# Optimization experiments

Hardware: AMD Instinct MI355X
Metric: run time of the kernel (lower is better)

The kernel has to match this reference:

```python
import jax, jax.numpy as jnp
import numpy as np

B, S, D = 4, 2048, 1024
H, HD = 16, 64  # num_heads, head_dim = qkv_features // num_heads


def setup_inputs() -> dict:
  key = jax.random.key(0)
  ks = jax.random.split(key, 11)
  s = 0.02
  return {
    'inputs_q': jax.random.normal(ks[0], (B, S, D), jnp.float32),
    'inputs_k': jax.random.normal(ks[1], (B, S, D), jnp.float32),
    'inputs_v': jax.random.normal(ks[2], (B, S, D), jnp.float32),
    # LinearGeneral kernels: [in_features, num_heads, head_dim]
    'Wq': jax.random.normal(ks[3], (D, H, HD), jnp.float32) * s,
    'bq': jnp.zeros((H, HD), jnp.float32),
    'Wk': jax.random.normal(ks[4], (D, H, HD), jnp.float32) * s,
    'bk': jnp.zeros((H, HD), jnp.float32),
    'Wv': jax.random.normal(ks[5], (D, H, HD), jnp.float32) * s,
    'bv': jnp.zeros((H, HD), jnp.float32),
    # output LinearGeneral kernel: [num_heads, head_dim, out_features]
    'Wo': jax.random.normal(ks[6], (H, HD, D), jnp.float32) * s,
    'bo': jnp.zeros((D,), jnp.float32),
  }


def reference(inputs_q, inputs_k, inputs_v, Wq, bq, Wk, bk, Wv, bv, Wo, bo):
  # q/k/v projections -> [B, S, H, HD]
  q = jnp.einsum('bsf,fhd->bshd', inputs_q, Wq) + bq
  k = jnp.einsum('bsf,fhd->bshd', inputs_k, Wk) + bk
  v = jnp.einsum('bsf,fhd->bshd', inputs_v, Wv) + bv
  # scaled dot-product attention (naive full softmax, as in the module)
  depth = q.shape[-1]
  q = q / jnp.sqrt(jnp.asarray(depth, q.dtype))
  attn = jnp.einsum('bqhd,bkhd->bhqk', q, k)  # [B, H, S, S]
  attn = jax.nn.softmax(attn, axis=-1)
  x = jnp.einsum('bhqk,bkhd->bqhd', attn, v)  # [B, S, H, HD]
  # output projection -> [B, S, D]
  out = jnp.einsum('bqhd,hdo->bqo', x, Wo) + bo
  return out
```

## Files before the change

kernel.cpp:

```cpp
#include <hip/hip_runtime.h>


typedef __attribute__((ext_vector_type(4))) float f32x4;
typedef __attribute__((ext_vector_type(8))) short short8;
typedef unsigned short u16;
typedef unsigned int u32;

__device__ __forceinline__ u16 f2bf(float f) {
  u32 u = __builtin_bit_cast(u32, f);
  u += 0x7fffu + ((u >> 16) & 1u);
  return (u16)(u >> 16);
}

__device__ __forceinline__ void gload16(const u16* g, u16* l) {
  __builtin_amdgcn_global_load_lds((const __attribute__((address_space(1))) void*)g,
                                   (__attribute__((address_space(3))) void*)l, 16, 0, 0);
}

__global__ __launch_bounds__(256) void cvt_f32_bf16_3(const float* __restrict__ a,
                                                      const float* __restrict__ b,
                                                      const float* __restrict__ c,
                                                      u16* __restrict__ oa,
                                                      u16* __restrict__ ob,
                                                      u16* __restrict__ oc) {
  const float* in = blockIdx.y == 0 ? a : (blockIdx.y == 1 ? b : c);
  u16* out = blockIdx.y == 0 ? oa : (blockIdx.y == 1 ? ob : oc);
  int i = blockIdx.x * 256 + threadIdx.x;
  float4 v = ((const float4*)in)[i];
  ushort4 o;
  o.x = f2bf(v.x); o.y = f2bf(v.y); o.z = f2bf(v.z); o.w = f2bf(v.w);
  ((ushort4*)out)[i] = o;
}

__global__ __launch_bounds__(256) void transpose_w4(const float* __restrict__ s0,
                                                    const float* __restrict__ s1,
                                                    const float* __restrict__ s2,
                                                    const float* __restrict__ s3,
                                                    u16* __restrict__ d0,
                                                    u16* __restrict__ d1,
                                                    u16* __restrict__ d2,
                                                    u16* __restrict__ d3) {
  const float* src = blockIdx.z == 0 ? s0 : (blockIdx.z == 1 ? s1 : (blockIdx.z == 2 ? s2 : s3));
  u16* dst = blockIdx.z == 0 ? d0 : (blockIdx.z == 1 ? d1 : (blockIdx.z == 2 ? d2 : d3));
  __shared__ float t[64][65];
  const int bx = blockIdx.x * 64;
  const int by = blockIdx.y * 64;
  const int tid = threadIdx.x;
  const int c4 = (tid & 15) * 4, r = tid >> 4;
#pragma unroll
  for (int i = 0; i < 4; ++i) {
    int row = r + i * 16;
    float4 v = *(const float4*)&src[(size_t)(by + row) * 1024 + bx + c4];
    t[row][c4] = v.x; t[row][c4 + 1] = v.y; t[row][c4 + 2] = v.z; t[row][c4 + 3] = v.w;
  }
  __syncthreads();
#pragma unroll
  for (int i = 0; i < 4; ++i) {
    int nrow = r + i * 16;
    ushort4 o;
    o.x = f2bf(t[c4 + 0][nrow]); o.y = f2bf(t[c4 + 1][nrow]);
    o.z = f2bf(t[c4 + 2][nrow]); o.w = f2bf(t[c4 + 3][nrow]);
    *(ushort4*)&dst[(size_t)(bx + nrow) * 1024 + by + c4] = o;
  }
}

template <int EPI>
__global__ __launch_bounds__(256) void gemm_k1024(const u16* __restrict__ A,
                                                  const u16* __restrict__ Bt,
                                                  const float* __restrict__ bias,
                                                  void* __restrict__ outp) {
  __shared__ u16 lds[2 * 8192];
  u16* ldsA = lds;
  u16* ldsB = lds + 8192;
  const int tid = threadIdx.x, ln = tid & 63, wv = tid >> 6;
  const int wr = wv >> 1, wc = wv & 1;
  const int lq = ln & 15, g = ln >> 4;
  const int m0 = blockIdx.y * 128, n0 = blockIdx.x * 128;
  f32x4 acc[4][4] = {};

  for (int kt = 0; kt < 16; ++kt) {
    const int k0 = kt * 64;
#pragma unroll
    for (int c = 0; c < 4; ++c) {
      int chunk = c * 256 + wv * 64 + ln;
      int row = chunk >> 3, cc = chunk & 7;
      gload16(A + (size_t)(m0 + row) * 1024 + k0 + ((cc ^ (row & 7)) << 3),
              ldsA + (c * 256 + wv * 64) * 8);
    }
#pragma unroll
    for (int c = 0; c < 4; ++c) {
      int chunk = c * 256 + wv * 64 + ln;
      int row = chunk >> 3, cc = chunk & 7;
      gload16(Bt + (size_t)(n0 + row) * 1024 + k0 + ((cc ^ (row & 7)) << 3),
              ldsB + (c * 256 + wv * 64) * 8);
    }
    __syncthreads();
#pragma unroll
    for (int ks = 0; ks < 2; ++ks) {
      short8 af[4], bf[4];
#pragma unroll
      for (int m = 0; m < 4; ++m) {
        int rA = wr * 64 + m * 16 + lq;
        int cc = (ks * 4 + g) ^ (rA & 7);
        af[m] = *(const short8*)&ldsA[rA * 64 + cc * 8];
      }
#pragma unroll
      for (int n = 0; n < 4; ++n) {
        int rB = wc * 64 + n * 16 + lq;
        int cc = (ks * 4 + g) ^ (rB & 7);
        bf[n] = *(const short8*)&ldsB[rB * 64 + cc * 8];
      }
#pragma unroll
      for (int m = 0; m < 4; ++m)
#pragma unroll
        for (int n = 0; n < 4; ++n)
          acc[m][n] = __builtin_amdgcn_mfma_f32_16x16x32_bf16(af[m], bf[n], acc[m][n], 0, 0, 0);
    }
    __syncthreads();
  }

#pragma unroll
  for (int m = 0; m < 4; ++m) {
#pragma unroll
    for (int n = 0; n < 4; ++n) {
      const int row = m0 + wr * 64 + m * 16 + g * 4;
      const int col = n0 + wc * 64 + n * 16 + lq;
      const float bb = bias[col];
      if constexpr (EPI == 0 || EPI == 1) {
        u16* O = (u16*)outp;
        int b = row >> 11, s = row & 2047, h = col >> 6, d = col & 63;
        size_t base = ((size_t)(b * 16 + h) * 2048 + s) * 64 + d;
#pragma unroll
        for (int j = 0; j < 4; ++j) {
          float v = acc[m][n][j] + bb;
          if constexpr (EPI == 0) v *= 0.18033688f;
          O[base + (size_t)j * 64] = f2bf(v);
        }
      } else if constexpr (EPI == 2) {
        u16* O = (u16*)outp;
        int b = row >> 11, s = row & 2047, h = col >> 6, d = col & 63;
        ushort4 pk;
        pk.x = f2bf(acc[m][n][0] + bb); pk.y = f2bf(acc[m][n][1] + bb);
        pk.z = f2bf(acc[m][n][2] + bb); pk.w = f2bf(acc[m][n][3] + bb);
        *(ushort4*)&O[((size_t)(b * 16 + h) * 64 + d) * 2048 + s] = pk;
      } else {
        float* O = (float*)outp;
#pragma unroll
        for (int j = 0; j < 4; ++j) O[(size_t)(row + j) * 1024 + col] = acc[m][n][j] + bb;
      }
    }
  }
}

__global__ __launch_bounds__(256) void attn_kernel(const u16* __restrict__ Q,
                                                   const u16* __restrict__ K,
                                                   const u16* __restrict__ Vt,
                                                   u16* __restrict__ Xat) {
  __shared__ u16 lds[4 * 4096 + 4 * 32 * 72];
  u16* ldsK0 = lds;
  u16* ldsK1 = lds + 4096;
  u16* ldsV0 = lds + 8192;
  u16* ldsV1 = lds + 12288;
  const int tid = threadIdx.x, ln = tid & 63, wv = tid >> 6;
  const int lq = ln & 15, g = ln >> 4;
  const int bh = blockIdx.y;
  const int q0 = blockIdx.x * 128 + wv * 32;
  u16* myP = lds + 16384 + wv * 32 * 72;

  const u16* Qb = Q + ((size_t)bh * 2048 + q0) * 64;
  const u16* Kb = K + (size_t)bh * 2048 * 64;
  const u16* Vb = Vt + (size_t)bh * 64 * 2048;

  short8 qf[2][2];
#pragma unroll
  for (int qb = 0; qb < 2; ++qb)
#pragma unroll
    for (int ks = 0; ks < 2; ++ks)
      qf[qb][ks] = *(const short8*)&Qb[(size_t)(qb * 16 + lq) * 64 + ks * 32 + g * 8];

  short8 ones;
#pragma unroll
  for (int i = 0; i < 8; ++i) ones[i] = (short)0x3F80;

  f32x4 accO[2][4] = {};
  f32x4 accL[2] = {};

  auto stage = [&](int s0, u16* dK, u16* dV) {
#pragma unroll
    for (int c = 0; c < 2; ++c) {
      int chunk = c * 256 + wv * 64 + ln;
      int row = chunk >> 3, cc = chunk & 7;
      gload16(Kb + (size_t)(s0 + row) * 64 + ((cc ^ (row & 7)) << 3),
              dK + (c * 256 + wv * 64) * 8);
    }
#pragma unroll
    for (int c = 0; c < 2; ++c) {
      int chunk = c * 256 + wv * 64 + ln;
      int row = chunk >> 3, cc = chunk & 7;
      gload16(Vb + (size_t)row * 2048 + s0 + ((cc ^ (row & 7)) << 3),
              dV + (c * 256 + wv * 64) * 8);
    }
  };

  auto compute = [&](const u16* cK, const u16* cV) {
    f32x4 accS[4][2] = {};
#pragma unroll
    for (int ks = 0; ks < 2; ++ks) {
      short8 kf[4];
#pragma unroll
      for (int m = 0; m < 4; ++m) {
        int r = m * 16 + lq;
        int cc = (ks * 4 + g) ^ (r & 7);
        kf[m] = *(const short8*)&cK[r * 64 + cc * 8];
      }
#pragma unroll
      for (int m = 0; m < 4; ++m)
#pragma unroll
        for (int qb = 0; qb < 2; ++qb)
          accS[m][qb] = __builtin_amdgcn_mfma_f32_16x16x32_bf16(kf[m], qf[qb][ks], accS[m][qb], 0, 0, 0);
    }
#pragma unroll
    for (int qb = 0; qb < 2; ++qb) {
      float p[16];
#pragma unroll
      for (int m = 0; m < 4; ++m)
#pragma unroll
        for (int j = 0; j < 4; ++j) p[m * 4 + j] = exp2f(accS[m][qb][j]);
#pragma unroll
      for (int m = 0; m < 4; ++m) {
        u32 w0, w1;
        asm("v_cvt_pk_bf16_f32 %0, %1, %2" : "=v"(w0) : "v"(p[m * 4 + 0]), "v"(p[m * 4 + 1]));
        asm("v_cvt_pk_bf16_f32 %0, %1, %2" : "=v"(w1) : "v"(p[m * 4 + 2]), "v"(p[m * 4 + 3]));
        uint2 w; w.x = w0; w.y = w1;
        *(uint2*)&myP[(qb * 16 + lq) * 72 + m * 16 + g * 4] = w;
      }
    }
#pragma unroll
    for (int ks = 0; ks < 2; ++ks) {
      short8 pf[2];
#pragma unroll
      for (int qb = 0; qb < 2; ++qb)
        pf[qb] = *(const short8*)&myP[(qb * 16 + lq) * 72 + ks * 32 + g * 8];
#pragma unroll
      for (int qb = 0; qb < 2; ++qb)
        accL[qb] = __builtin_amdgcn_mfma_f32_16x16x32_bf16(pf[qb], ones, accL[qb], 0, 0, 0);
#pragma unroll
      for (int n = 0; n < 4; ++n) {
        int r = n * 16 + lq;
        int cc = (ks * 4 + g) ^ (r & 7);
        short8 vf = *(const short8*)&cV[r * 64 + cc * 8];
#pragma unroll
        for (int qb = 0; qb < 2; ++qb)
          accO[qb][n] = __builtin_amdgcn_mfma_f32_16x16x32_bf16(pf[qb], vf, accO[qb][n], 0, 0, 0);
      }
    }
  };

  stage(0, ldsK0, ldsV0);

  for (int t = 0; t < 16; ++t) {
    const int kv0 = 2 * t;
    stage((kv0 + 1) * 64, ldsK1, ldsV1);
    asm volatile("s_waitcnt vmcnt(4)" ::: "memory");
    __builtin_amdgcn_s_barrier();
    __builtin_amdgcn_sched_barrier(0);
    compute(ldsK0, ldsV0);
    __builtin_amdgcn_s_barrier();
    __builtin_amdgcn_sched_barrier(0);
    if (t < 15) {
      stage((kv0 + 2) * 64, ldsK0, ldsV0);
      asm volatile("s_waitcnt vmcnt(4)" ::: "memory");
    } else {
      asm volatile("s_waitcnt vmcnt(0)" ::: "memory");
    }
    __builtin_amdgcn_s_barrier();
    __builtin_amdgcn_sched_barrier(0);
    compute(ldsK1, ldsV1);
    __builtin_amdgcn_s_barrier();
    __builtin_amdgcn_sched_barrier(0);
  }

  const int b = bh >> 4, h = bh & 15;
#pragma unroll
  for (int qb = 0; qb < 2; ++qb) {
    float inv_row[4];
#pragma unroll
    for (int j = 0; j < 4; ++j) inv_row[j] = 1.0f / accL[qb][j];
#pragma unroll
    for (int n = 0; n < 4; ++n)
#pragma unroll
      for (int j = 0; j < 4; ++j) {
        int s = q0 + qb * 16 + g * 4 + j;
        Xat[((size_t)b * 2048 + s) * 1024 + h * 64 + n * 16 + lq] = f2bf(accO[qb][n][j] * inv_row[j]);
      }
  }
}

extern "C" void kernel_launch(void* const* d_in, const int* in_sizes, int n_in,
                              void* d_out, int out_size, void* d_ws, size_t ws_size,
                              hipStream_t stream) {
  const float* xq = (const float*)d_in[0];
  const float* xk = (const float*)d_in[1];
  const float* xv = (const float*)d_in[2];
  const float* Wq = (const float*)d_in[3];
  const float* bq = (const float*)d_in[4];
  const float* Wk = (const float*)d_in[5];
  const float* bk = (const float*)d_in[6];
  const float* Wv = (const float*)d_in[7];
  const float* bv = (const float*)d_in[8];
  const float* Wo = (const float*)d_in[9];
  const float* bo = (const float*)d_in[10];

  char* ws = (char*)d_ws;
  u16* Xqb = (u16*)(ws + 0);
  u16* Xkb = (u16*)(ws + 16777216);
  u16* Xvb = (u16*)(ws + 33554432);
  u16* Wtq = (u16*)(ws + 50331648);
  u16* Wtk = (u16*)(ws + 52428800);
  u16* Wtv = (u16*)(ws + 54525952);
  u16* Wot = (u16*)(ws + 56623104);
  u16* Qb  = (u16*)(ws + 58720256);
  u16* Kb  = (u16*)(ws + 75497472);
  u16* Vtb = (u16*)(ws + 92274688);
  u16* Xat = Xqb;

  cvt_f32_bf16_3<<<dim3(8192, 3), 256, 0, stream>>>(xq, xk, xv, Xqb, Xkb, Xvb);
  transpose_w4<<<dim3(16, 16, 4), 256, 0, stream>>>(Wq, Wk, Wv, Wo, Wtq, Wtk, Wtv, Wot);

  gemm_k1024<0><<<dim3(8, 64), 256, 0, stream>>>(Xqb, Wtq, bq, Qb);
  gemm_k1024<1><<<dim3(8, 64), 256, 0, stream>>>(Xkb, Wtk, bk, Kb);
  gemm_k1024<2><<<dim3(8, 64), 256, 0, stream>>>(Xvb, Wtv, bv, Vtb);

  attn_kernel<<<dim3(16, 64), 256, 0, stream>>>(Qb, Kb, Vtb, Xat);

  gemm_k1024<3><<<dim3(8, 64), 256, 0, stream>>>(Xat, Wot, bo, d_out);
}
```

Baseline: 378.6 us.

## Merge QKV GEMMs, swizzle blocks across XCDs, widen attention blocks, add setprio

The three QKV projection GEMMs become one launch indexed by blockIdx.z, and the GEMM tiles are remapped so that blocks on the same XCD share A rows for L2 reuse. Attention now uses 512-thread blocks covering 256 queries, so each K/V tile staged in LDS serves twice as many queries, with one load per thread and the waitcnt adjusted to match. The MFMA sections are wrapped in s_setprio and exp2f is replaced with a raw v_exp_f32. The risks are lower occupancy from the larger attention block and the looser accuracy of v_exp_f32 compared with exp2f.

```diff
diff --git a/kernel.cpp b/kernel.cpp
--- a/kernel.cpp
+++ b/kernel.cpp
@@ -10,6 +10,12 @@
   u32 u = __builtin_bit_cast(u32, f);
   u += 0x7fffu + ((u >> 16) & 1u);
   return (u16)(u >> 16);
+}
+
+__device__ __forceinline__ float fast_exp2(float x) {
+  float r;
+  asm("v_exp_f32 %0, %1" : "=v"(r) : "v"(x));
+  return r;
 }
 
 __device__ __forceinline__ void gload16(const u16* g, u16* l) {
@@ -64,19 +70,21 @@
   }
 }
 
-template <int EPI>
-__global__ __launch_bounds__(256) void gemm_k1024(const u16* __restrict__ A,
-                                                  const u16* __restrict__ Bt,
-                                                  const float* __restrict__ bias,
-                                                  void* __restrict__ outp) {
-  __shared__ u16 lds[2 * 8192];
-  u16* ldsA = lds;
-  u16* ldsB = lds + 8192;
-  const int tid = threadIdx.x, ln = tid & 63, wv = tid >> 6;
+__device__ __forceinline__ void xcd_swizzle(int& m0, int& n0) {
+  int flat = blockIdx.y * 8 + blockIdx.x;
+  int xcd = flat & 7, j = flat >> 3;
+  m0 = ((xcd << 3) + (j >> 3)) * 128;
+  n0 = (j & 7) * 128;
+}
+
+__device__ __forceinline__ void gemm_core(const u16* __restrict__ A,
+                                          const u16* __restrict__ Bt,
+                                          u16* ldsA, u16* ldsB,
+                                          int m0, int n0, int tid,
+                                          f32x4 (&acc)[4][4]) {
+  const int ln = tid & 63, wv = tid >> 6;
   const int wr = wv >> 1, wc = wv & 1;
   const int lq = ln & 15, g = ln >> 4;
-  const int m0 = blockIdx.y * 128, n0 = blockIdx.x * 128;
-  f32x4 acc[4][4] = {};
 
   for (int kt = 0; kt < 16; ++kt) {
     const int k0 = kt * 64;
@@ -110,15 +118,46 @@
         int cc = (ks * 4 + g) ^ (rB & 7);
         bf[n] = *(const short8*)&ldsB[rB * 64 + cc * 8];
       }
+      __builtin_amdgcn_s_setprio(1);
 #pragma unroll
       for (int m = 0; m < 4; ++m)
 #pragma unroll
         for (int n = 0; n < 4; ++n)
           acc[m][n] = __builtin_amdgcn_mfma_f32_16x16x32_bf16(af[m], bf[n], acc[m][n], 0, 0, 0);
+      __builtin_amdgcn_s_setprio(0);
     }
     __syncthreads();
   }
-
+}
+
+__global__ __launch_bounds__(256) void gemm_qkv(const u16* __restrict__ Aq,
+                                                const u16* __restrict__ Ak,
+                                                const u16* __restrict__ Av,
+                                                const u16* __restrict__ Btq,
+                                                const u16* __restrict__ Btk,
+                                                const u16* __restrict__ Btv,
+                                                const float* __restrict__ bq,
+                                                const float* __restrict__ bk,
+                                                const float* __restrict__ bv,
+                                                u16* __restrict__ Oq,
+                                                u16* __restrict__ Ok,
+                                                u16* __restrict__ Ov) {
+  __shared__ u16 lds[2 * 8192];
+  const int z = blockIdx.z;
+  const u16* A = z == 0 ? Aq : (z == 1 ? Ak : Av);
+  const u16* Bt = z == 0 ? Btq : (z == 1 ? Btk : Btv);
+  const float* bias = z == 0 ? bq : (z == 1 ? bk : bv);
+  u16* O = z == 0 ? Oq : (z == 1 ? Ok : Ov);
+
+  int m0, n0;
+  xcd_swizzle(m0, n0);
+  const int tid = threadIdx.x, ln = tid & 63, wv = tid >> 6;
+  const int wr = wv >> 1, wc = wv & 1;
+  const int lq = ln & 15, g = ln >> 4;
+  f32x4 acc[4][4] = {};
+  gemm_core(A, Bt, lds, lds + 8192, m0, n0, tid, acc);
+
+  const float scl = (z == 0) ? 0.18033688f : 1.0f;
 #pragma unroll
   for (int m = 0; m < 4; ++m) {
 #pragma unroll
@@ -126,37 +165,51 @@
       const int row = m0 + wr * 64 + m * 16 + g * 4;
       const int col = n0 + wc * 64 + n * 16 + lq;
       const float bb = bias[col];
-      if constexpr (EPI == 0 || EPI == 1) {
-        u16* O = (u16*)outp;
-        int b = row >> 11, s = row & 2047, h = col >> 6, d = col & 63;
+      int b = row >> 11, s = row & 2047, h = col >> 6, d = col & 63;
+      if (z < 2) {
         size_t base = ((size_t)(b * 16 + h) * 2048 + s) * 64 + d;
 #pragma unroll
-        for (int j = 0; j < 4; ++j) {
-          float v = acc[m][n][j] + bb;
-          if constexpr (EPI == 0) v *= 0.18033688f;
-          O[base + (size_t)j * 64] = f2bf(v);
-        }
-      } else if constexpr (EPI == 2) {
-        u16* O = (u16*)outp;
-        int b = row >> 11, s = row & 2047, h = col >> 6, d = col & 63;
+        for (int j = 0; j < 4; ++j)
+          O[base + (size_t)j * 64] = f2bf((acc[m][n][j] + bb) * scl);
+      } else {
         ushort4 pk;
         pk.x = f2bf(acc[m][n][0] + bb); pk.y = f2bf(acc[m][n][1] + bb);
         pk.z = f2bf(acc[m][n][2] + bb); pk.w = f2bf(acc[m][n][3] + bb);
         *(ushort4*)&O[((size_t)(b * 16 + h) * 64 + d) * 2048 + s] = pk;
-      } else {
-        float* O = (float*)outp;
-#pragma unroll
-        for (int j = 0; j < 4; ++j) O[(size_t)(row + j) * 1024 + col] = acc[m][n][j] + bb;
-      }
-    }
-  }
-}
-
-__global__ __launch_bounds__(256) void attn_kernel(const u16* __restrict__ Q,
+      }
+    }
+  }
+}
+
+__global__ __launch_bounds__(256) void gemm_out(const u16* __restrict__ A,
+                                                const u16* __restrict__ Bt,
+                                                const float* __restrict__ bias,
+                                                float* __restrict__ O) {
+  __shared__ u16 lds[2 * 8192];
+  int m0, n0;
+  xcd_swizzle(m0, n0);
+  const int tid = threadIdx.x, ln = tid & 63, wv = tid >> 6;
+  const int wr = wv >> 1, wc = wv & 1;
+  const int lq = ln & 15, g = ln >> 4;
+  f32x4 acc[4][4] = {};
+  gemm_core(A, Bt, lds, lds + 8192, m0, n0, tid, acc);
+#pragma unroll
+  for (int m = 0; m < 4; ++m)
+#pragma unroll
+    for (int n = 0; n < 4; ++n) {
+      const int row = m0 + wr * 64 + m * 16 + g * 4;
+      const int col = n0 + wc * 64 + n * 16 + lq;
+      const float bb = bias[col];
+#pragma unroll
+      for (int j = 0; j < 4; ++j) O[(size_t)(row + j) * 1024 + col] = acc[m][n][j] + bb;
+    }
+}
+
+__global__ __launch_bounds__(512) void attn_kernel(const u16* __restrict__ Q,
                                                    const u16* __restrict__ K,
                                                    const u16* __restrict__ Vt,
                                                    u16* __restrict__ Xat) {
-  __shared__ u16 lds[4 * 4096 + 4 * 32 * 72];
+  __shared__ u16 lds[4 * 4096 + 8 * 32 * 72];
   u16* ldsK0 = lds;
   u16* ldsK1 = lds + 4096;
   u16* ldsV0 = lds + 8192;
@@ -164,7 +217,7 @@
   const int tid = threadIdx.x, ln = tid & 63, wv = tid >> 6;
   const int lq = ln & 15, g = ln >> 4;
   const int bh = blockIdx.y;
-  const int q0 = blockIdx.x * 128 + wv * 32;
+  const int q0 = blockIdx.x * 256 + wv * 32;
   u16* myP = lds + 16384 + wv * 32 * 72;
 
   const u16* Qb = Q + ((size_t)bh * 2048 + q0) * 64;
@@ -186,20 +239,10 @@
   f32x4 accL[2] = {};
 
   auto stage = [&](int s0, u16* dK, u16* dV) {
-#pragma unroll
-    for (int c = 0; c < 2; ++c) {
-      int chunk = c * 256 + wv * 64 + ln;
-      int row = chunk >> 3, cc = chunk & 7;
-      gload16(Kb + (size_t)(s0 + row) * 64 + ((cc ^ (row & 7)) << 3),
-              dK + (c * 256 + wv * 64) * 8);
-    }
-#pragma unroll
-    for (int c = 0; c < 2; ++c) {
-      int chunk = c * 256 + wv * 64 + ln;
-      int row = chunk >> 3, cc = chunk & 7;
-      gload16(Vb + (size_t)row * 2048 + s0 + ((cc ^ (row & 7)) << 3),
-              dV + (c * 256 + wv * 64) * 8);
-    }
+    int chunk = wv * 64 + ln;
+    int row = chunk >> 3, cc = chunk & 7;
+    gload16(Kb + (size_t)(s0 + row) * 64 + ((cc ^ (row & 7)) << 3), dK + wv * 512);
+    gload16(Vb + (size_t)row * 2048 + s0 + ((cc ^ (row & 7)) << 3), dV + wv * 512);
   };
 
   auto compute = [&](const u16* cK, const u16* cV) {
@@ -213,11 +256,13 @@
         int cc = (ks * 4 + g) ^ (r & 7);
         kf[m] = *(const short8*)&cK[r * 64 + cc * 8];
       }
+      __builtin_amdgcn_s_setprio(1);
 #pragma unroll
       for (int m = 0; m < 4; ++m)
 #pragma unroll
         for (int qb = 0; qb < 2; ++qb)
           accS[m][qb] = __builtin_amdgcn_mfma_f32_16x16x32_bf16(kf[m], qf[qb][ks], accS[m][qb], 0, 0, 0);
+      __builtin_amdgcn_s_setprio(0);
     }
 #pragma unroll
     for (int qb = 0; qb < 2; ++qb) {
@@ -225,7 +270,7 @@
 #pragma unroll
       for (int m = 0; m < 4; ++m)
 #pragma unroll
-        for (int j = 0; j < 4; ++j) p[m * 4 + j] = exp2f(accS[m][qb][j]);
+        for (int j = 0; j < 4; ++j) p[m * 4 + j] = fast_exp2(accS[m][qb][j]);
 #pragma unroll
       for (int m = 0; m < 4; ++m) {
         u32 w0, w1;
@@ -249,9 +294,11 @@
         int r = n * 16 + lq;
         int cc = (ks * 4 + g) ^ (r & 7);
         short8 vf = *(const short8*)&cV[r * 64 + cc * 8];
+        __builtin_amdgcn_s_setprio(1);
 #pragma unroll
         for (int qb = 0; qb < 2; ++qb)
           accO[qb][n] = __builtin_amdgcn_mfma_f32_16x16x32_bf16(pf[qb], vf, accO[qb][n], 0, 0, 0);
+        __builtin_amdgcn_s_setprio(0);
       }
     }
   };
@@ -261,7 +308,7 @@
   for (int t = 0; t < 16; ++t) {
     const int kv0 = 2 * t;
     stage((kv0 + 1) * 64, ldsK1, ldsV1);
-    asm volatile("s_waitcnt vmcnt(4)" ::: "memory");
+    asm volatile("s_waitcnt vmcnt(2)" ::: "memory");
     __builtin_amdgcn_s_barrier();
     __builtin_amdgcn_sched_barrier(0);
     compute(ldsK0, ldsV0);
@@ -269,7 +316,7 @@
     __builtin_amdgcn_sched_barrier(0);
     if (t < 15) {
       stage((kv0 + 2) * 64, ldsK0, ldsV0);
-      asm volatile("s_waitcnt vmcnt(4)" ::: "memory");
+      asm volatile("s_waitcnt vmcnt(2)" ::: "memory");
     } else {
       asm volatile("s_waitcnt vmcnt(0)" ::: "memory");
     }
@@ -327,11 +374,10 @@
   cvt_f32_bf16_3<<<dim3(8192, 3), 256, 0, stream>>>(xq, xk, xv, Xqb, Xkb, Xvb);
   transpose_w4<<<dim3(16, 16, 4), 256, 0, stream>>>(Wq, Wk, Wv, Wo, Wtq, Wtk, Wtv, Wot);
 
-  gemm_k1024<0><<<dim3(8, 64), 256, 0, stream>>>(Xqb, Wtq, bq, Qb);
-  gemm_k1024<1><<<dim3(8, 64), 256, 0, stream>>>(Xkb, Wtk, bk, Kb);
-  gemm_k1024<2><<<dim3(8, 64), 256, 0, stream>>>(Xvb, Wtv, bv, Vtb);
-
-  attn_kernel<<<dim3(16, 64), 256, 0, stream>>>(Qb, Kb, Vtb, Xat);
-
-  gemm_k1024<3><<<dim3(8, 64), 256, 0, stream>>>(Xat, Wot, bo, d_out);
-}
+  gemm_qkv<<<dim3(8, 64, 3), 256, 0, stream>>>(Xqb, Xkb, Xvb, Wtq, Wtk, Wtv,
+                                               bq, bk, bv, Qb, Kb, Vtb);
+
+  attn_kernel<<<dim3(8, 64), 512, 0, stream>>>(Qb, Kb, Vtb, Xat);
+
+  gemm_out<<<dim3(8, 64), 256, 0, stream>>>(Xat, Wot, bo, (float*)d_out);
+}
```

New measurement: 334.9 us. -11.6%, faster.
